# Kernel optimization log

Hardware: AMD Instinct MI355X
Metric: run time of the kernel (lower is better)

The kernel has to match this reference:

```python
import jax, jax.numpy as jnp
import numpy as np

INPUT_SIZE = 512
HIDDEN_SIZE = 1024
SEQ_LEN = 512
BATCH = 64

def _xavier(key, shape):
    fan_out, fan_in = shape
    bound = float(np.sqrt(6.0 / (fan_in + fan_out)))
    return jax.random.uniform(key, shape, jnp.float32, -bound, bound)

def setup_inputs() -> dict:
    key = jax.random.key(0)
    ks = jax.random.split(key, 5)
    return {
        "x_seq": jax.random.normal(ks[0], (SEQ_LEN, BATCH, INPUT_SIZE), jnp.float32),
        "h0": jax.random.normal(ks[1], (BATCH, HIDDEN_SIZE), jnp.float32),
        "U_c": _xavier(ks[2], (HIDDEN_SIZE, INPUT_SIZE)),
        "w_c": jnp.ones((HIDDEN_SIZE,), jnp.float32),
        "b_c": jnp.zeros((HIDDEN_SIZE,), jnp.float32),
        "U_a": _xavier(ks[3], (HIDDEN_SIZE, INPUT_SIZE)),
        "w_a": jnp.ones((HIDDEN_SIZE,), jnp.float32),
        "b_a": jnp.zeros((HIDDEN_SIZE,), jnp.float32),
        "U_h": _xavier(ks[4], (HIDDEN_SIZE, INPUT_SIZE)),
        "b_h": jnp.zeros((HIDDEN_SIZE,), jnp.float32),
    }

def reference(x_seq, h0, U_c, w_c, b_c, U_a, w_a, b_a, U_h, b_h):
    # Batch the three input projections across all timesteps (the compute-heavy
    # GEMMs), then run the inherently-sequential gated recurrence with lax.scan.
    xc = jnp.einsum('tbi,hi->tbh', x_seq, U_c) + b_c  # [T, B, H]
    xa = jnp.einsum('tbi,hi->tbh', x_seq, U_a) + b_a
    xh = jnp.einsum('tbi,hi->tbh', x_seq, U_h) + b_h

    def step(h, proj):
        pc, pa, ph = proj
        c = jax.nn.sigmoid(pc + w_c * h)
        a = 1.0 + jnp.tanh(pa + w_a * h)
        h_new = c * h + (1.0 - c) * jnp.tanh(ph + a * h)
        return h_new, h_new

    h_last, y_seq = jax.lax.scan(step, h0, (xc, xa, xh))
    return (y_seq, (h_last,))
```

## Files before the change

kernel.cpp:

```cpp
#include <hip/hip_runtime.h>
#include <cstdint>
#include <cstddef>

#define T_SEQ 512
#define BATCH 64
#define IN_SZ 512
#define HID   1024
#define BH    (BATCH*HID)
#define M_TOT (T_SEQ*BATCH)
#define D_CH  16

typedef float f32x4 __attribute__((ext_vector_type(4)));
typedef _Float16 f16x8 __attribute__((ext_vector_type(8)));

__device__ inline unsigned short f2h(float f){
  union { _Float16 h; unsigned short u; } v;
  v.h = (_Float16)f;
  return v.u;
}
__device__ inline float h2f(unsigned short s){
  union { unsigned short u; _Float16 h; } v; v.u = s;
  return (float)v.h;
}

__device__ inline float sigm_f(float x){ return 1.f/(1.f + __expf(-x)); }
__device__ inline float tanh_f(float x){ float e = __expf(2.f*x); return 1.f - 2.f/(e + 1.f); }

__device__ inline void async16(const void* g, void* l){
  __builtin_amdgcn_global_load_lds(
      (__attribute__((address_space(1))) void*)g,
      (__attribute__((address_space(3))) void*)l,
      16, 0, 0);
}

#define XBLK 16384
__global__ __launch_bounds__(256) void cvt_all(
    const float* __restrict__ x,  const float* __restrict__ Uc,
    const float* __restrict__ Ua, const float* __restrict__ Uh,
    unsigned short* __restrict__ xb, unsigned short* __restrict__ U0,
    unsigned short* __restrict__ U1, unsigned short* __restrict__ U2)
{
  int b = blockIdx.x;
  const float* in; unsigned short* out; int i;
  if (b < XBLK){
    in = x; out = xb; i = b*256 + threadIdx.x;
  } else {
    int r = b - XBLK;
    int which = r >> 9;
    int lb = r & 511;
    i = lb*256 + threadIdx.x;
    in  = (which==0) ? Uc : (which==1) ? Ua : Uh;
    out = (which==0) ? U0 : (which==1) ? U1 : U2;
  }
  float4 v = ((const float4*)in)[i];
  ushort4 o;
  o.x = f2h(v.x); o.y = f2h(v.y); o.z = f2h(v.z); o.w = f2h(v.w);
  ((ushort4*)out)[i] = o;
}

__global__ __launch_bounds__(512, 2) void gemm3(
    const unsigned short* __restrict__ xb,
    const unsigned short* __restrict__ U0,
    const unsigned short* __restrict__ U1,
    const unsigned short* __restrict__ U2,
    const float* __restrict__ b0, const float* __restrict__ b1, const float* __restrict__ b2,
    unsigned short* out0, unsigned short* out1, void* out2, int ph_f16)
{
  __shared__ __align__(16) unsigned char smem_raw[131072];

  const int tid  = threadIdx.x;
  const int wave = tid >> 6, lane = tid & 63;
  const int quad = lane >> 4, l16 = lane & 15;

  const int bid  = blockIdx.x;
  const int xcd  = bid & 7;
  const int slot = bid >> 3;
  const int mbl  = slot / 12;
  const int inner= slot - mbl*12;
  const int mb   = xcd*16 + mbl;
  const int z    = inner % 3;
  const int nb   = inner / 3;

  const int m0 = mb * 256, n0 = nb * 256;
  const unsigned short* Um = (z==0) ? U0 : (z==1) ? U1 : U2;
  const float* bias        = (z==0) ? b0 : (z==1) ? b1 : b2;
  const int wm = wave >> 2, wn = wave & 3;

  const int laneRow = lane >> 2;
  const int cg8     = ((lane & 3) ^ ((lane >> 3) & 3)) << 3;
  const unsigned short* srcA = xb + (size_t)m0 * IN_SZ;
  const unsigned short* srcB = Um + (size_t)n0 * IN_SZ;

  const int cxa = l16*64 + ((quad ^ ((l16 >> 1) & 3)) << 4);

  auto stageA = [&](int tile, int kh){
    unsigned char* dst = smem_raw + (((tile & 1)*2 + kh) << 14);
#pragma unroll
    for (int j = 0; j < 2; ++j){
      const unsigned short* g = srcA + (size_t)((wave*2 + j)*16 + laneRow)*IN_SZ
                                + tile*64 + kh*32 + cg8;
      async16(g, dst + (wave*2 + j)*1024);
    }
  };
  auto stageB = [&](int tile, int kh){
    unsigned char* dst = smem_raw + 65536 + (((tile & 1)*2 + kh) << 14);
#pragma unroll
    for (int j = 0; j < 2; ++j){
      const unsigned short* g = srcB + (size_t)((wave*2 + j)*16 + laneRow)*IN_SZ
                                + tile*64 + kh*32 + cg8;
      async16(g, dst + (wave*2 + j)*1024);
    }
  };

  const f32x4 zf = {0.f, 0.f, 0.f, 0.f};
  f32x4 acc[8][4];
#pragma unroll
  for (int i = 0; i < 8; ++i)
#pragma unroll
    for (int j = 0; j < 4; ++j) acc[i][j] = zf;

  stageA(0,0); stageB(0,0); stageA(0,1); stageB(0,1);
  stageA(1,0); stageB(1,0); stageA(1,1);
  asm volatile("s_waitcnt vmcnt(10)" ::: "memory");
  __builtin_amdgcn_s_barrier();

#define CLUSTER(B0_, B1_, N0_, N1_)                                                      \
  __builtin_amdgcn_s_barrier();                                                          \
  asm volatile("s_waitcnt lgkmcnt(0)" ::: "memory");                                     \
  __builtin_amdgcn_s_setprio(1);                                                         \
  _Pragma("unroll")                                                                      \
  for (int im_ = 0; im_ < 8; ++im_){                                                     \
    acc[im_][N0_] = __builtin_amdgcn_mfma_f32_16x16x32_f16(a0[im_], B0_, acc[im_][N0_], 0,0,0); \
    acc[im_][N1_] = __builtin_amdgcn_mfma_f32_16x16x32_f16(a0[im_], B1_, acc[im_][N1_], 0,0,0); \
  }                                                                                      \
  __builtin_amdgcn_s_setprio(0);                                                         \
  __builtin_amdgcn_s_barrier();

  f16x8 a0[8];
#pragma unroll
  for (int g = 0; g < 8; ++g){
    const int buf = g & 1;
    const unsigned char* Ab0 = smem_raw + ((buf*2 + 0) << 14);
    const unsigned char* Ab1 = smem_raw + ((buf*2 + 1) << 14);
    const unsigned char* Bb0 = smem_raw + 65536 + ((buf*2 + 0) << 14);
    const unsigned char* Bb1 = smem_raw + 65536 + ((buf*2 + 1) << 14);

#pragma unroll
    for (int im = 0; im < 8; ++im)
      a0[im] = *(const f16x8*)(Ab0 + wm*8192 + im*1024 + cxa);
    f16x8 q0 = *(const f16x8*)(Bb0 + wn*4096 + 0*1024 + cxa);
    f16x8 q1 = *(const f16x8*)(Bb0 + wn*4096 + 1*1024 + cxa);
    if (g < 7) stageB(g+1, 1);
    CLUSTER(q0, q1, 0, 1)

    f16x8 q2 = *(const f16x8*)(Bb0 + wn*4096 + 2*1024 + cxa);
    f16x8 q3 = *(const f16x8*)(Bb0 + wn*4096 + 3*1024 + cxa);
    if (g < 6) stageA(g+2, 0);
    if (g < 6)      { asm volatile("s_waitcnt vmcnt(10)" ::: "memory"); }
    else if (g == 6){ asm volatile("s_waitcnt vmcnt(8)"  ::: "memory"); }
    else            { asm volatile("s_waitcnt vmcnt(0)"  ::: "memory"); }
    CLUSTER(q2, q3, 2, 3)

#pragma unroll
    for (int im = 0; im < 8; ++im)
      a0[im] = *(const f16x8*)(Ab1 + wm*8192 + im*1024 + cxa);
    q0 = *(const f16x8*)(Bb1 + wn*4096 + 0*1024 + cxa);
    q1 = *(const f16x8*)(Bb1 + wn*4096 + 1*1024 + cxa);
    if (g < 6) stageB(g+2, 0);
    CLUSTER(q0, q1, 0, 1)

    q2 = *(const f16x8*)(Bb1 + wn*4096 + 2*1024 + cxa);
    q3 = *(const f16x8*)(Bb1 + wn*4096 + 3*1024 + cxa);
    if (g < 6) stageA(g+2, 1);
    if (g < 6)      { asm volatile("s_waitcnt vmcnt(10)" ::: "memory"); }
    else if (g == 6){ asm volatile("s_waitcnt vmcnt(4)"  ::: "memory"); }
    CLUSTER(q2, q3, 2, 3)
  }
#undef CLUSTER

  float bv[4];
#pragma unroll
  for (int in = 0; in < 4; ++in) bv[in] = bias[n0 + wn*64 + in*16 + l16];

  if (z == 2 && !ph_f16) {
    float* o32 = (float*)out2;
#pragma unroll
    for (int im = 0; im < 8; ++im)
#pragma unroll
      for (int r = 0; r < 4; ++r){
        int grow = m0 + wm*128 + im*16 + quad*4 + r;
        size_t rb = (size_t)grow * HID;
#pragma unroll
        for (int in = 0; in < 4; ++in)
          o32[rb + n0 + wn*64 + in*16 + l16] = acc[im][in][r] + bv[in];
      }
    return;
  }

  unsigned short* op = (z==0) ? out0 : (z==1) ? out1 : (unsigned short*)out2;
  unsigned short* sw = (unsigned short*)smem_raw + wave*4608;
#pragma unroll
  for (int h = 0; h < 2; ++h){
#pragma unroll
    for (int i4 = 0; i4 < 4; ++i4){
      int im = h*4 + i4;
#pragma unroll
      for (int r = 0; r < 4; ++r){
        int lr = i4*16 + quad*4 + r;
#pragma unroll
        for (int in = 0; in < 4; ++in)
          sw[lr*72 + in*16 + l16] = f2h(acc[im][in][r] + bv[in]);
      }
    }
    asm volatile("s_waitcnt lgkmcnt(0)" ::: "memory");
#pragma unroll
    for (int i = 0; i < 8; ++i){
      int lr = i*8 + (lane >> 3);
      int ch = lane & 7;
      uint4 v = *(const uint4*)(sw + lr*72 + ch*8);
      int grow = m0 + wm*128 + h*64 + lr;
      *(uint4*)(op + (size_t)grow*HID + n0 + wn*64 + ch*8) = v;
    }
    if (h == 0) asm volatile("s_waitcnt lgkmcnt(0)" ::: "memory");
  }
}

template <bool PH16>
__global__ __launch_bounds__(256) void scan_k(
    const unsigned short* __restrict__ pc, const unsigned short* __restrict__ pa,
    const void* __restrict__ phv,
    float* __restrict__ y,
    const float* __restrict__ h0, const float* __restrict__ wc, const float* __restrict__ wa,
    float* __restrict__ hlast)
{
  const int idx  = blockIdx.x * 256 + threadIdx.x;
  const int hidx = idx & (HID - 1);
  float h = h0[idx];
  const float wcv = wc[hidx], wav = wa[hidx];
  const unsigned short* ph16 = (const unsigned short*)phv;
  const float*          ph32 = (const float*)phv;

  unsigned short cpc[D_CH], cpa[D_CH];
  unsigned short npc[D_CH], npa[D_CH];
  float cph[D_CH], nph[D_CH];
  unsigned short cph16[D_CH], nph16[D_CH];

#pragma unroll
  for (int i = 0; i < D_CH; i++){
    size_t b = (size_t)i*BH + idx;
    cpc[i] = pc[b]; cpa[i] = pa[b];
    if (PH16) cph16[i] = ph16[b]; else cph[i] = ph32[b];
  }

  constexpr int NC = T_SEQ / D_CH;
  for (int c = 0; c < NC; c++){
    const int t0 = c * D_CH;
    if (c + 1 < NC){
#pragma unroll
      for (int i = 0; i < D_CH; i++){
        size_t b = (size_t)(t0 + D_CH + i)*BH + idx;
        npc[i] = pc[b]; npa[i] = pa[b];
        if (PH16) nph16[i] = ph16[b]; else nph[i] = ph32[b];
      }
    }
#pragma unroll
    for (int i = 0; i < D_CH; i++){
      float pcv = h2f(cpc[i]);
      float pav = h2f(cpa[i]);
      float phv_ = PH16 ? h2f(cph16[i]) : cph[i];
      float cc = sigm_f(pcv + wcv*h);
      float a  = 1.f + tanh_f(pav + wav*h);
      float hc = tanh_f(phv_ + a*h);
      h = cc*h + (1.f - cc)*hc;
      y[(size_t)(t0 + i)*BH + idx] = h;
    }
    if (c + 1 < NC){
#pragma unroll
      for (int i = 0; i < D_CH; i++){
        cpc[i] = npc[i]; cpa[i] = npa[i];
        if (PH16) cph16[i] = nph16[i]; else cph[i] = nph[i];
      }
    }
  }
  hlast[idx] = h;
}

extern "C" void kernel_launch(void* const* d_in, const int* in_sizes, int n_in,
                              void* d_out, int out_size, void* d_ws, size_t ws_size,
                              hipStream_t stream)
{
  const float* x  = (const float*)d_in[0];
  const float* h0 = (const float*)d_in[1];
  const float* Uc = (const float*)d_in[2];
  const float* wc = (const float*)d_in[3];
  const float* bc = (const float*)d_in[4];
  const float* Ua = (const float*)d_in[5];
  const float* wa = (const float*)d_in[6];
  const float* ba = (const float*)d_in[7];
  const float* Uh = (const float*)d_in[8];
  const float* bh = (const float*)d_in[9];

  float* y     = (float*)d_out;
  float* hlast = y + (size_t)T_SEQ * BH;

  const size_t szP16 = (size_t)T_SEQ * BH * 2;
  const size_t szX16 = (size_t)M_TOT * IN_SZ * 2;
  const size_t szU16 = (size_t)HID * IN_SZ * 2;

  const size_t base = 2*szP16 + szX16 + 3*szU16;
  const bool ph_sep = ws_size >= base + szP16;

  char* w = (char*)d_ws;
  unsigned short* pc16 = (unsigned short*)w;
  unsigned short* pa16 = (unsigned short*)(w + szP16);
  unsigned short* xb   = (unsigned short*)(w + 2*szP16);
  unsigned short* U0b  = (unsigned short*)(w + 2*szP16 + szX16);
  unsigned short* U1b  = U0b + szU16/2;
  unsigned short* U2b  = U1b + szU16/2;
  unsigned short* ph16 = (unsigned short*)(w + base);

  cvt_all<<<XBLK + 3*512, 256, 0, stream>>>(x, Uc, Ua, Uh, xb, U0b, U1b, U2b);

  void* phbuf = ph_sep ? (void*)ph16 : (void*)y;
  gemm3<<<1536, 512, 0, stream>>>(xb, U0b, U1b, U2b, bc, ba, bh,
                                  pc16, pa16, phbuf, ph_sep ? 1 : 0);

  if (ph_sep)
    scan_k<true><<<BH/256, 256, 0, stream>>>(pc16, pa16, (const void*)ph16,
                                             y, h0, wc, wa, hlast);
  else
    scan_k<false><<<BH/256, 256, 0, stream>>>(pc16, pa16, (const void*)y,
                                              y, h0, wc, wa, hlast);
}
```

Measured before the change: 414.6 us.

## Stage scan projections through LDS with async double-buffered loads

The scan kernel no longer prefetches projection chunks into per-thread register arrays. It now issues async 16-byte global-to-LDS copies into double-buffered shared memory, waits with vmcnt and a barrier, and reads each timestep's values from LDS. The goal is wider, coalesced loads and lower register pressure, which should allow better latency hiding. In exchange the kernel uses 64KB of LDS per block, which limits occupancy, adds block-level barriers, and depends on a hand-counted vmcnt(16) that also has to account for the y stores.

```diff
diff --git a/kernel.cpp b/kernel.cpp
--- a/kernel.cpp
+++ b/kernel.cpp
@@ -233,53 +233,79 @@
     const float* __restrict__ h0, const float* __restrict__ wc, const float* __restrict__ wa,
     float* __restrict__ hlast)
 {
-  const int idx  = blockIdx.x * 256 + threadIdx.x;
+  __shared__ __align__(16) unsigned char sm[65536];
+  const int tid  = threadIdx.x;
+  const int wave = tid >> 6, lane = tid & 63;
+  const int col0 = blockIdx.x * 256;
+  const int idx  = col0 + tid;
   const int hidx = idx & (HID - 1);
+
   float h = h0[idx];
   const float wcv = wc[hidx], wav = wa[hidx];
   const unsigned short* ph16 = (const unsigned short*)phv;
   const float*          ph32 = (const float*)phv;
 
-  unsigned short cpc[D_CH], cpa[D_CH];
-  unsigned short npc[D_CH], npa[D_CH];
-  float cph[D_CH], nph[D_CH];
-  unsigned short cph16[D_CH], nph16[D_CH];
-
-#pragma unroll
-  for (int i = 0; i < D_CH; i++){
-    size_t b = (size_t)i*BH + idx;
-    cpc[i] = pc[b]; cpa[i] = pa[b];
-    if (PH16) cph16[i] = ph16[b]; else cph[i] = ph32[b];
-  }
+  unsigned char* pcL = sm;
+  unsigned char* paL = sm + 16384;
+  unsigned char* phL = sm + 32768;
+
+  auto stage = [&](int c){
+    const int b  = c & 1;
+    const int t0 = c * D_CH;
+#pragma unroll
+    for (int j = 0; j < 2; ++j){
+      const int tr  = wave*2 + j*8;
+      const int row = tr + (lane >> 5);
+      const int ce  = (lane & 31) * 8;
+      async16(pc + (size_t)(t0+row)*BH + col0 + ce, pcL + b*8192 + tr*512);
+      async16(pa + (size_t)(t0+row)*BH + col0 + ce, paL + b*8192 + tr*512);
+    }
+    if (PH16){
+#pragma unroll
+      for (int j = 0; j < 2; ++j){
+        const int tr  = wave*2 + j*8;
+        const int row = tr + (lane >> 5);
+        const int ce  = (lane & 31) * 8;
+        async16(ph16 + (size_t)(t0+row)*BH + col0 + ce, phL + b*8192 + tr*512);
+      }
+    } else {
+#pragma unroll
+      for (int j = 0; j < 4; ++j){
+        const int t = wave + j*4;
+        async16(ph32 + (size_t)(t0+t)*BH + col0 + lane*4, phL + b*16384 + t*1024);
+      }
+    }
+  };
+
+  stage(0);
+  asm volatile("s_waitcnt vmcnt(0)" ::: "memory");
+  __builtin_amdgcn_s_barrier();
+  __builtin_amdgcn_sched_barrier(0);
 
   constexpr int NC = T_SEQ / D_CH;
-  for (int c = 0; c < NC; c++){
+  for (int c = 0; c < NC; ++c){
+    if (c + 1 < NC) stage(c + 1);
+    const int b  = c & 1;
     const int t0 = c * D_CH;
-    if (c + 1 < NC){
-#pragma unroll
-      for (int i = 0; i < D_CH; i++){
-        size_t b = (size_t)(t0 + D_CH + i)*BH + idx;
-        npc[i] = pc[b]; npa[i] = pa[b];
-        if (PH16) nph16[i] = ph16[b]; else nph[i] = ph32[b];
-      }
-    }
-#pragma unroll
-    for (int i = 0; i < D_CH; i++){
-      float pcv = h2f(cpc[i]);
-      float pav = h2f(cpa[i]);
-      float phv_ = PH16 ? h2f(cph16[i]) : cph[i];
+    const unsigned short* pcb   = (const unsigned short*)(pcL + b*8192)  + tid;
+    const unsigned short* pab   = (const unsigned short*)(paL + b*8192)  + tid;
+    const unsigned short* phb16 = (const unsigned short*)(phL + b*8192)  + tid;
+    const float*          phb32 = (const float*)(phL + b*16384) + tid;
+#pragma unroll
+    for (int i = 0; i < D_CH; ++i){
+      float pcv = h2f(pcb[i*256]);
+      float pav = h2f(pab[i*256]);
+      float ph_ = PH16 ? h2f(phb16[i*256]) : phb32[i*256];
       float cc = sigm_f(pcv + wcv*h);
       float a  = 1.f + tanh_f(pav + wav*h);
-      float hc = tanh_f(phv_ + a*h);
+      float hc = tanh_f(ph_ + a*h);
       h = cc*h + (1.f - cc)*hc;
       y[(size_t)(t0 + i)*BH + idx] = h;
     }
     if (c + 1 < NC){
-#pragma unroll
-      for (int i = 0; i < D_CH; i++){
-        cpc[i] = npc[i]; cpa[i] = npa[i];
-        if (PH16) cph16[i] = nph16[i]; else cph[i] = nph[i];
-      }
+      asm volatile("s_waitcnt vmcnt(16)" ::: "memory");
+      __builtin_amdgcn_s_barrier();
+      __builtin_amdgcn_sched_barrier(0);
     }
   }
   hlast[idx] = h;
```

Result: faster. 372.2 us (-10.2%).
